# Performance work log

Hardware: AMD Instinct MI355X
Metric: run time of the kernel (lower is better)

Reference implementation:

```python
import jax, jax.numpy as jnp
import numpy as np

FG_FRACTION = 0.5
BATCHSIZE = 256
NUM_IMAGES = 1
NUM_CLASSES = 21
FG_THRESH = 0.5
BG_THRESH_HI = 0.5
BG_THRESH_LO = 0.1
ROIS_PER_IMAGE = BATCHSIZE // NUM_IMAGES                      # 256
FG_ROIS_PER_IMAGE = int(round(FG_FRACTION * ROIS_PER_IMAGE))  # 128
BG_ROIS_PER_IMAGE = ROIS_PER_IMAGE - FG_ROIS_PER_IMAGE        # 128


def _make_boxes(key, n, img=1000.0, max_wh=200.0):
    k1, k2 = jax.random.split(key)
    xy = jax.random.uniform(k1, (n, 2), dtype=jnp.float32) * (img - max_wh)
    wh = jax.random.uniform(k2, (n, 2), dtype=jnp.float32) * max_wh + 1.0
    return jnp.concatenate([xy, xy + wh], axis=1)  # valid [x1,y1,x2,y2]


def setup_inputs() -> dict:
    key = jax.random.key(0)
    k1, k2, k3 = jax.random.split(key, 3)
    N, G = 250000, 128
    rois = _make_boxes(k1, N)
    all_rois = jnp.concatenate([jnp.zeros((N, 1), jnp.float32), rois], axis=1)  # [N,5], col0 = image idx
    gt_boxes = _make_boxes(k2, G)                                               # [G,4]
    gt_labels = jax.random.randint(k3, (G,), 1, NUM_CLASSES).astype(jnp.int32)  # fg classes 1..20
    return {"all_rois": all_rois, "gt_boxes": gt_boxes, "gt_labels": gt_labels}


def _iou(a, b):
    area_a = (a[:, 2] - a[:, 0] + 1.0) * (a[:, 3] - a[:, 1] + 1.0)
    area_b = (b[:, 2] - b[:, 0] + 1.0) * (b[:, 3] - b[:, 1] + 1.0)
    ix1 = jnp.maximum(a[:, None, 0], b[None, :, 0])
    iy1 = jnp.maximum(a[:, None, 1], b[None, :, 1])
    ix2 = jnp.minimum(a[:, None, 2], b[None, :, 2])
    iy2 = jnp.minimum(a[:, None, 3], b[None, :, 3])
    iw = jnp.clip(ix2 - ix1 + 1.0, 0.0)
    ih = jnp.clip(iy2 - iy1 + 1.0, 0.0)
    inter = iw * ih
    return inter / (area_a[:, None] + area_b[None, :] - inter)


def _bbox_transform(ex, gt):
    ew = ex[:, 2] - ex[:, 0] + 1.0
    eh = ex[:, 3] - ex[:, 1] + 1.0
    ecx = ex[:, 0] + 0.5 * ew
    ecy = ex[:, 1] + 0.5 * eh
    gw = gt[:, 2] - gt[:, 0] + 1.0
    gh = gt[:, 3] - gt[:, 1] + 1.0
    gcx = gt[:, 0] + 0.5 * gw
    gcy = gt[:, 1] + 0.5 * gh
    return jnp.stack([(gcx - ecx) / ew, (gcy - ecy) / eh,
                      jnp.log(gw / ew), jnp.log(gh / eh)], axis=1)


def _proposal_target(all_rois, gt_boxes, gt_labels):
    G = gt_boxes.shape[0]
    # append gt boxes (with image-index 0 column) to the proposal set
    gt_rois = jnp.concatenate([jnp.zeros((G, 1), all_rois.dtype), gt_boxes], axis=1)
    all_rois = jnp.concatenate([all_rois, gt_rois], axis=0)          # [N+G, 5]

    overlaps = _iou(all_rois[:, 1:5], gt_boxes)                       # [N+G, G] -- dominant memory traffic
    gt_assignment = jnp.argmax(overlaps, axis=1)                      # [N+G]
    max_ov = jnp.max(overlaps, axis=1)                                # [N+G]
    labels_all = gt_labels[gt_assignment]                             # [N+G]

    fg_mask = max_ov >= FG_THRESH
    bg_mask = (max_ov < BG_THRESH_HI) & (max_ov >= BG_THRESH_LO)

    # random fg/bg sampling: top-k over random keys restricted to each mask
    u = jax.random.uniform(jax.random.key(42), (all_rois.shape[0],), dtype=jnp.float32)
    fg_idx = jax.lax.top_k(jnp.where(fg_mask, u, -1.0), FG_ROIS_PER_IMAGE)[1]
    bg_idx = jax.lax.top_k(jnp.where(bg_mask, u, -1.0), BG_ROIS_PER_IMAGE)[1]
    keep = jnp.concatenate([fg_idx, bg_idx])                          # [256]

    valid_fg = fg_mask[fg_idx]  # if fewer fg than requested, pad slots get label 0
    labels = jnp.concatenate([jnp.where(valid_fg, labels_all[fg_idx], 0),
                              jnp.zeros((BG_ROIS_PER_IMAGE,), labels_all.dtype)])

    rois = all_rois[keep]                                             # [256, 5]
    targets = _bbox_transform(rois[:, 1:5], gt_boxes[gt_assignment[keep]])  # [256, 4]

    # scatter targets into class-specific columns [256, 4*num_classes]
    onehot = jax.nn.one_hot(labels, NUM_CLASSES, dtype=targets.dtype)
    bbox_targets = (onehot[:, :, None] * targets[:, None, :]).reshape(ROIS_PER_IMAGE, 4 * NUM_CLASSES)
    bbox_targets = bbox_targets * (labels > 0)[:, None].astype(targets.dtype)
    return rois, labels, bbox_targets


def reference(all_rois, gt_boxes, gt_labels):
    return _proposal_target(all_rois, gt_boxes, gt_labels)
```

## Files before the change

kernel.cpp:

```cpp
#include <hip/hip_runtime.h>
#include <stdint.h>

#define GMAX 128
#define TK 128
#define NBINS 4096
#define CAND_MAX 4096
#define NUM_CLASSES 21
#define CBLOCK 1024
#define CBLOCKS 62

__device__ __forceinline__ void threefry2x32(uint32_t k0, uint32_t k1,
                                             uint32_t& x0, uint32_t& x1) {
  uint32_t ks0 = k0, ks1 = k1, ks2 = k0 ^ k1 ^ 0x1BD11BDAu;
  x0 += ks0; x1 += ks1;
#define TF_ROUND(r) { x0 += x1; x1 = (x1 << (r)) | (x1 >> (32 - (r))); x1 ^= x0; }
  TF_ROUND(13) TF_ROUND(15) TF_ROUND(26) TF_ROUND(6)
  x0 += ks1; x1 += ks2 + 1u;
  TF_ROUND(17) TF_ROUND(29) TF_ROUND(16) TF_ROUND(24)
  x0 += ks2; x1 += ks0 + 2u;
  TF_ROUND(13) TF_ROUND(15) TF_ROUND(26) TF_ROUND(6)
  x0 += ks0; x1 += ks1 + 3u;
  TF_ROUND(17) TF_ROUND(29) TF_ROUND(16) TF_ROUND(24)
  x0 += ks1; x1 += ks2 + 4u;
  TF_ROUND(13) TF_ROUND(15) TF_ROUND(26) TF_ROUND(6)
  x0 += ks2; x1 += ks0 + 5u;
#undef TF_ROUND
}

__global__ void __launch_bounds__(256)
score_kernel(const float* __restrict__ all_rois,
             const float* __restrict__ gt_boxes,
             uint32_t* __restrict__ score,
             uint32_t* __restrict__ hist,
             int N, int M, int G) {
  __shared__ float4 sbox[GMAX];
  __shared__ float  sga[GMAX];
  const int t = threadIdx.x;
  if (t < G) {
    float4 b = reinterpret_cast<const float4*>(gt_boxes)[t];
    sbox[t] = b;
    sga[t] = __fmul_rn(__fadd_rn(__fsub_rn(b.z, b.x), 1.0f),
                       __fadd_rn(__fsub_rn(b.w, b.y), 1.0f));
  }
  __syncthreads();
  const int i = blockIdx.x * 256 + t;
  if (i >= M) return;

  float bx1, by1, bx2, by2;
  if (i < N) {
    bx1 = all_rois[(size_t)i * 5 + 1];
    by1 = all_rois[(size_t)i * 5 + 2];
    bx2 = all_rois[(size_t)i * 5 + 3];
    by2 = all_rois[(size_t)i * 5 + 4];
  } else {
    float4 b = sbox[i - N];
    bx1 = b.x; by1 = b.y; bx2 = b.z; by2 = b.w;
  }
  const float area = __fmul_rn(__fadd_rn(__fsub_rn(bx2, bx1), 1.0f),
                               __fadd_rn(__fsub_rn(by2, by1), 1.0f));
  float best = -1.0f;
  int bi = 0;
  for (int g = 0; g < G; ++g) {
    float4 gb = sbox[g];
    float ix1 = fmaxf(bx1, gb.x);
    float iy1 = fmaxf(by1, gb.y);
    float ix2 = fminf(bx2, gb.z);
    float iy2 = fminf(by2, gb.w);
    float iw = fmaxf(__fadd_rn(__fsub_rn(ix2, ix1), 1.0f), 0.0f);
    float ih = fmaxf(__fadd_rn(__fsub_rn(iy2, iy1), 1.0f), 0.0f);
    float inter = __fmul_rn(iw, ih);
    float uni = __fsub_rn(__fadd_rn(area, sga[g]), inter);
    float ov = __fdiv_rn(inter, uni);
    if (ov > best) { best = ov; bi = g; }
  }

  uint32_t cx0 = 0u, cx1 = (uint32_t)i;
  threefry2x32(0u, 42u, cx0, cx1);
  uint32_t ubits = (cx0 ^ cx1) >> 9;

  uint32_t fg = (best >= 0.5f) ? 1u : 0u;
  uint32_t bg = (!fg && best >= 0.1f) ? 1u : 0u;
  score[i] = (ubits << 9) | ((uint32_t)bi << 2) | (fg << 1) | bg;
  if (fg)      atomicAdd(&hist[ubits >> 11], 1u);
  else if (bg) atomicAdd(&hist[NBINS + (ubits >> 11)], 1u);
}

__global__ void __launch_bounds__(CBLOCK)
compact_kernel(const uint32_t* __restrict__ score, int M,
               const uint32_t* __restrict__ hist,
               int* __restrict__ meta_cnt,
               uint64_t* __restrict__ cand) {
  __shared__ uint64_t gs[CBLOCK];
  __shared__ int s_jstar[2], s_bth[2];
  const int t = threadIdx.x;

  {
    const int b0 = 4 * t;
    uint64_t acc = 0;
    for (int k = 0; k < 4; ++k)
      acc += ((uint64_t)hist[b0 + k] << 32) | (uint64_t)hist[NBINS + b0 + k];
    gs[t] = acc;
    if (t < 2) s_jstar[t] = -1;
    __syncthreads();
    for (int d = 1; d < CBLOCK; d <<= 1) {
      uint64_t add = (t + d < CBLOCK) ? gs[t + d] : 0ull;
      __syncthreads();
      gs[t] += add;
      __syncthreads();
    }
    uint32_t vfg = (uint32_t)(gs[t] >> 32);
    uint32_t vbg = (uint32_t)gs[t];
    uint32_t nfg = (t < CBLOCK - 1) ? (uint32_t)(gs[t + 1] >> 32) : 0u;
    uint32_t nbg = (t < CBLOCK - 1) ? (uint32_t)gs[t + 1] : 0u;
    if (vfg >= (uint32_t)TK && (t == CBLOCK - 1 || nfg < (uint32_t)TK)) s_jstar[0] = t;
    if (vbg >= (uint32_t)TK && (t == CBLOCK - 1 || nbg < (uint32_t)TK)) s_jstar[1] = t;
    __syncthreads();
    if (t == 0) {
      for (int m = 0; m < 2; ++m) {
        int j = s_jstar[m], B = -1;
        if (j >= 0) {
          uint32_t base = 0;
          if (j < CBLOCK - 1)
            base = (m == 0) ? (uint32_t)(gs[j + 1] >> 32) : (uint32_t)gs[j + 1];
          const uint32_t* h = hist + m * NBINS;
          B = 4 * j;
          for (int b = 4 * j + 3; b >= 4 * j; --b) {
            base += h[b];
            if (base >= (uint32_t)TK) { B = b; break; }
          }
        }
        s_bth[m] = B;
      }
    }
    __syncthreads();
  }

  for (int i = blockIdx.x * CBLOCK + t; i < M; i += CBLOCKS * CBLOCK) {
    uint32_t s = score[i];
    uint32_t mb = s & 3u;
    if (!mb) continue;
    int m = (mb & 2u) ? 0 : 1;
    int B = s_bth[m];
    if (B >= 0 && (int)(s >> 20) < B) continue;
    int p = atomicAdd(&meta_cnt[m], 1);
    if (p < CAND_MAX)
      cand[(size_t)m * CAND_MAX + p] =
          (((uint64_t)((s >> 9) + 1u)) << 32) | (uint64_t)(~(uint32_t)i);
  }
}

__global__ void __launch_bounds__(1024)
final_kernel(const float* __restrict__ all_rois,
             const float* __restrict__ gt_boxes,
             const int* __restrict__ gt_labels,
             const uint32_t* __restrict__ score,
             const uint64_t* __restrict__ cand_g,
             const int* __restrict__ meta_cnt,
             float* __restrict__ out, int N, int M) {
  __shared__ uint64_t cand[CAND_MAX];
  __shared__ int keep[2 * TK];
  __shared__ int fgvalid[TK];
  __shared__ float s_tx[2 * TK], s_ty[2 * TK], s_tw[2 * TK], s_th[2 * TK];
  __shared__ int s_label[2 * TK];
  const int t = threadIdx.x;

  for (int m = 0; m < 2; ++m) {
    int cnt = meta_cnt[m]; if (cnt > CAND_MAX) cnt = CAND_MAX;
    int P = TK;
    while (P < cnt) P <<= 1;
    for (int p = t; p < P; p += 1024)
      cand[p] = (p < cnt) ? cand_g[(size_t)m * CAND_MAX + p] : 0ull;
    __syncthreads();
    for (int k = 2; k <= P; k <<= 1) {
      for (int j = k >> 1; j > 0; j >>= 1) {
        for (int idx = t; idx < P; idx += 1024) {
          int l = idx ^ j;
          if (l > idx) {
            uint64_t a = cand[idx], b = cand[l];
            bool swp = ((idx & k) == 0) ? (a < b) : (a > b);
            if (swp) { cand[idx] = b; cand[l] = a; }
          }
        }
        __syncthreads();
      }
    }
    if (cnt < TK && t == 0) {
      int fill = cnt;
      uint32_t mask_bit = (m == 0) ? 2u : 1u;
      for (int i = 0; i < M && fill < TK; ++i)
        if (!(score[i] & mask_bit)) cand[fill++] = (uint64_t)(~(uint32_t)i);
    }
    __syncthreads();
    if (t < TK) {
      uint64_t c = cand[t];
      keep[m * TK + t] = (int)(~(uint32_t)(c & 0xFFFFFFFFull));
      if (m == 0) fgvalid[t] = ((c >> 32) != 0ull) ? 1 : 0;
    }
    __syncthreads();
  }

  const int R = 2 * TK;
  float* rois_out   = out;
  float* labels_out = out + (size_t)R * 5;
  float* bt_out     = out + (size_t)R * 5 + R;

  if (t < R) {
    const int i = keep[t];
    float rimg, rx1, ry1, rx2, ry2;
    if (i < N) {
      rimg = all_rois[(size_t)i * 5 + 0];
      rx1  = all_rois[(size_t)i * 5 + 1];
      ry1  = all_rois[(size_t)i * 5 + 2];
      rx2  = all_rois[(size_t)i * 5 + 3];
      ry2  = all_rois[(size_t)i * 5 + 4];
    } else {
      int g = i - N;
      rimg = 0.0f;
      rx1 = gt_boxes[g * 4 + 0]; ry1 = gt_boxes[g * 4 + 1];
      rx2 = gt_boxes[g * 4 + 2]; ry2 = gt_boxes[g * 4 + 3];
    }
    rois_out[t * 5 + 0] = rimg;
    rois_out[t * 5 + 1] = rx1;
    rois_out[t * 5 + 2] = ry1;
    rois_out[t * 5 + 3] = rx2;
    rois_out[t * 5 + 4] = ry2;

    const int ga = (int)((score[i] >> 2) & 127u);
    int label = (t < TK && fgvalid[t]) ? gt_labels[ga] : 0;
    labels_out[t] = (float)label;
    s_label[t] = label;

    float gx1 = gt_boxes[ga * 4 + 0], gy1 = gt_boxes[ga * 4 + 1];
    float gx2 = gt_boxes[ga * 4 + 2], gy2 = gt_boxes[ga * 4 + 3];
    float ew = rx2 - rx1 + 1.0f, eh = ry2 - ry1 + 1.0f;
    float ecx = rx1 + 0.5f * ew, ecy = ry1 + 0.5f * eh;
    float gw = gx2 - gx1 + 1.0f, gh = gy2 - gy1 + 1.0f;
    float gcx = gx1 + 0.5f * gw, gcy = gy1 + 0.5f * gh;
    s_tx[t] = (gcx - ecx) / ew;
    s_ty[t] = (gcy - ecy) / eh;
    s_tw[t] = logf(gw / ew);
    s_th[t] = logf(gh / eh);
  }
  __syncthreads();

  const int TOT = R * 4 * NUM_CLASSES;
  for (int idx = t; idx < TOT; idx += 1024) {
    int r = idx / (4 * NUM_CLASSES);
    int c = idx - r * (4 * NUM_CLASSES);
    int lab = s_label[r];
    float v = 0.0f;
    if (lab > 0 && (c >> 2) == lab) {
      int cc = c & 3;
      v = (cc == 0) ? s_tx[r] : (cc == 1) ? s_ty[r] : (cc == 2) ? s_tw[r] : s_th[r];
    }
    bt_out[idx] = v;
  }
}

extern "C" void kernel_launch(void* const* d_in, const int* in_sizes, int n_in,
                              void* d_out, int out_size, void* d_ws, size_t ws_size,
                              hipStream_t stream) {
  const float* all_rois = (const float*)d_in[0];
  const float* gt_boxes = (const float*)d_in[1];
  const int*   gt_labels = (const int*)d_in[2];
  const int N = in_sizes[0] / 5;
  const int G = in_sizes[2];
  const int M = N + G;

  char* ws = (char*)d_ws;
  int* meta = (int*)ws;
  uint32_t* hist = (uint32_t*)(ws + 256);
  size_t off = 256 + (size_t)2 * NBINS * 4;
  uint32_t* score = (uint32_t*)(ws + off);
  off += (((size_t)M * 4) + 255) & ~(size_t)255;
  uint64_t* cand = (uint64_t*)(ws + off);
  float* out = (float*)d_out;

  hipMemsetAsync(ws, 0, 256 + (size_t)2 * NBINS * 4, stream);
  score_kernel<<<(M + 255) / 256, 256, 0, stream>>>(all_rois, gt_boxes, score,
                                                    hist, N, M, G);
  compact_kernel<<<CBLOCKS, CBLOCK, 0, stream>>>(score, M, hist, meta, cand);
  final_kernel<<<1, 1024, 0, stream>>>(all_rois, gt_boxes, gt_labels, score,
                                       cand, meta, out, N, M);
}
```

Baseline: 116.2 us.

## Fold histogram threshold into last score block; rank-select candidates instead of bitonic sort

The histogram prefix scan and threshold-bin search move out of the compact kernel into the last-finishing block of the score kernel, found through an atomic block counter, and the thresholds are written to global metadata. The compact kernel becomes a wide 256-thread grid that reads four scores per thread with vectorized loads and no per-block prologue scan. The final kernel replaces the shared-memory bitonic sort with a quadratic rank count per candidate, cutting the barrier-heavy sort passes. The trade-offs are an extra atomic and fence per score block and O(cnt^2) rank work, which relies on the candidate count staying small.

```diff
diff --git a/kernel.cpp b/kernel.cpp
--- a/kernel.cpp
+++ b/kernel.cpp
@@ -6,8 +6,6 @@
 #define NBINS 4096
 #define CAND_MAX 4096
 #define NUM_CLASSES 21
-#define CBLOCK 1024
-#define CBLOCKS 62
 
 __device__ __forceinline__ void threefry2x32(uint32_t k0, uint32_t k1,
                                              uint32_t& x0, uint32_t& x1) {
@@ -32,6 +30,7 @@
              const float* __restrict__ gt_boxes,
              uint32_t* __restrict__ score,
              uint32_t* __restrict__ hist,
+             int* __restrict__ meta,
              int N, int M, int G) {
   __shared__ float4 sbox[GMAX];
   __shared__ float  sga[GMAX];
@@ -44,108 +43,128 @@
   }
   __syncthreads();
   const int i = blockIdx.x * 256 + t;
-  if (i >= M) return;
-
-  float bx1, by1, bx2, by2;
-  if (i < N) {
-    bx1 = all_rois[(size_t)i * 5 + 1];
-    by1 = all_rois[(size_t)i * 5 + 2];
-    bx2 = all_rois[(size_t)i * 5 + 3];
-    by2 = all_rois[(size_t)i * 5 + 4];
+
+  if (i < M) {
+    float bx1, by1, bx2, by2;
+    if (i < N) {
+      bx1 = all_rois[(size_t)i * 5 + 1];
+      by1 = all_rois[(size_t)i * 5 + 2];
+      bx2 = all_rois[(size_t)i * 5 + 3];
+      by2 = all_rois[(size_t)i * 5 + 4];
+    } else {
+      float4 b = sbox[i - N];
+      bx1 = b.x; by1 = b.y; bx2 = b.z; by2 = b.w;
+    }
+    const float area = __fmul_rn(__fadd_rn(__fsub_rn(bx2, bx1), 1.0f),
+                                 __fadd_rn(__fsub_rn(by2, by1), 1.0f));
+    float best = -1.0f;
+    int bi = 0;
+    for (int g = 0; g < G; ++g) {
+      float4 gb = sbox[g];
+      float ix1 = fmaxf(bx1, gb.x);
+      float iy1 = fmaxf(by1, gb.y);
+      float ix2 = fminf(bx2, gb.z);
+      float iy2 = fminf(by2, gb.w);
+      float iw = fmaxf(__fadd_rn(__fsub_rn(ix2, ix1), 1.0f), 0.0f);
+      float ih = fmaxf(__fadd_rn(__fsub_rn(iy2, iy1), 1.0f), 0.0f);
+      float inter = __fmul_rn(iw, ih);
+      float uni = __fsub_rn(__fadd_rn(area, sga[g]), inter);
+      float ov = __fdiv_rn(inter, uni);
+      if (ov > best) { best = ov; bi = g; }
+    }
+
+    uint32_t cx0 = 0u, cx1 = (uint32_t)i;
+    threefry2x32(0u, 42u, cx0, cx1);
+    uint32_t ubits = (cx0 ^ cx1) >> 9;
+
+    uint32_t fg = (best >= 0.5f) ? 1u : 0u;
+    uint32_t bg = (!fg && best >= 0.1f) ? 1u : 0u;
+    score[i] = (ubits << 9) | ((uint32_t)bi << 2) | (fg << 1) | bg;
+    if (fg)      atomicAdd(&hist[ubits >> 11], 1u);
+    else if (bg) atomicAdd(&hist[NBINS + (ubits >> 11)], 1u);
+  }
+
+  __threadfence();
+  __shared__ unsigned s_prev;
+  if (t == 0) s_prev = atomicAdd((unsigned int*)&meta[2], 1u);
+  __syncthreads();
+  if (s_prev != gridDim.x - 1) return;
+  __threadfence();
+
+  __shared__ uint64_t gs[256];
+  __shared__ int s_jstar[2];
+  const int b0 = 16 * t;
+  uint64_t acc = 0;
+  for (int k = 0; k < 16; ++k) {
+    uint32_t hf = __hip_atomic_load(&hist[b0 + k], __ATOMIC_RELAXED,
+                                    __HIP_MEMORY_SCOPE_AGENT);
+    uint32_t hb = __hip_atomic_load(&hist[NBINS + b0 + k], __ATOMIC_RELAXED,
+                                    __HIP_MEMORY_SCOPE_AGENT);
+    acc += ((uint64_t)hf << 32) | (uint64_t)hb;
+  }
+  gs[t] = acc;
+  if (t < 2) s_jstar[t] = -1;
+  __syncthreads();
+  for (int d = 1; d < 256; d <<= 1) {
+    uint64_t add = (t + d < 256) ? gs[t + d] : 0ull;
+    __syncthreads();
+    gs[t] += add;
+    __syncthreads();
+  }
+  uint32_t vfg = (uint32_t)(gs[t] >> 32);
+  uint32_t vbg = (uint32_t)gs[t];
+  uint32_t nfg = (t < 255) ? (uint32_t)(gs[t + 1] >> 32) : 0u;
+  uint32_t nbg = (t < 255) ? (uint32_t)gs[t + 1] : 0u;
+  if (vfg >= (uint32_t)TK && (t == 255 || nfg < (uint32_t)TK)) s_jstar[0] = t;
+  if (vbg >= (uint32_t)TK && (t == 255 || nbg < (uint32_t)TK)) s_jstar[1] = t;
+  __syncthreads();
+  if (t == 0) {
+    for (int m = 0; m < 2; ++m) {
+      int j = s_jstar[m], B = -1;
+      if (j >= 0) {
+        uint32_t base = 0;
+        if (j < 255)
+          base = (m == 0) ? (uint32_t)(gs[j + 1] >> 32) : (uint32_t)gs[j + 1];
+        B = 16 * j;
+        for (int b = 16 * j + 15; b >= 16 * j; --b) {
+          base += __hip_atomic_load(&hist[m * NBINS + b], __ATOMIC_RELAXED,
+                                    __HIP_MEMORY_SCOPE_AGENT);
+          if (base >= (uint32_t)TK) { B = b; break; }
+        }
+      }
+      meta[4 + m] = B;
+    }
+  }
+}
+
+__global__ void __launch_bounds__(256)
+compact_kernel(const uint32_t* __restrict__ score, int M,
+               int* __restrict__ meta,
+               uint64_t* __restrict__ cand) {
+  const int bth[2] = {meta[4], meta[5]};
+  const int base = (blockIdx.x * 256 + threadIdx.x) * 4;
+  if (base >= M) return;
+  uint32_t ss[4];
+  int lim;
+  if (base + 3 < M) {
+    uint4 s4 = *reinterpret_cast<const uint4*>(score + base);
+    ss[0] = s4.x; ss[1] = s4.y; ss[2] = s4.z; ss[3] = s4.w;
+    lim = 4;
   } else {
-    float4 b = sbox[i - N];
-    bx1 = b.x; by1 = b.y; bx2 = b.z; by2 = b.w;
-  }
-  const float area = __fmul_rn(__fadd_rn(__fsub_rn(bx2, bx1), 1.0f),
-                               __fadd_rn(__fsub_rn(by2, by1), 1.0f));
-  float best = -1.0f;
-  int bi = 0;
-  for (int g = 0; g < G; ++g) {
-    float4 gb = sbox[g];
-    float ix1 = fmaxf(bx1, gb.x);
-    float iy1 = fmaxf(by1, gb.y);
-    float ix2 = fminf(bx2, gb.z);
-    float iy2 = fminf(by2, gb.w);
-    float iw = fmaxf(__fadd_rn(__fsub_rn(ix2, ix1), 1.0f), 0.0f);
-    float ih = fmaxf(__fadd_rn(__fsub_rn(iy2, iy1), 1.0f), 0.0f);
-    float inter = __fmul_rn(iw, ih);
-    float uni = __fsub_rn(__fadd_rn(area, sga[g]), inter);
-    float ov = __fdiv_rn(inter, uni);
-    if (ov > best) { best = ov; bi = g; }
-  }
-
-  uint32_t cx0 = 0u, cx1 = (uint32_t)i;
-  threefry2x32(0u, 42u, cx0, cx1);
-  uint32_t ubits = (cx0 ^ cx1) >> 9;
-
-  uint32_t fg = (best >= 0.5f) ? 1u : 0u;
-  uint32_t bg = (!fg && best >= 0.1f) ? 1u : 0u;
-  score[i] = (ubits << 9) | ((uint32_t)bi << 2) | (fg << 1) | bg;
-  if (fg)      atomicAdd(&hist[ubits >> 11], 1u);
-  else if (bg) atomicAdd(&hist[NBINS + (ubits >> 11)], 1u);
-}
-
-__global__ void __launch_bounds__(CBLOCK)
-compact_kernel(const uint32_t* __restrict__ score, int M,
-               const uint32_t* __restrict__ hist,
-               int* __restrict__ meta_cnt,
-               uint64_t* __restrict__ cand) {
-  __shared__ uint64_t gs[CBLOCK];
-  __shared__ int s_jstar[2], s_bth[2];
-  const int t = threadIdx.x;
-
-  {
-    const int b0 = 4 * t;
-    uint64_t acc = 0;
-    for (int k = 0; k < 4; ++k)
-      acc += ((uint64_t)hist[b0 + k] << 32) | (uint64_t)hist[NBINS + b0 + k];
-    gs[t] = acc;
-    if (t < 2) s_jstar[t] = -1;
-    __syncthreads();
-    for (int d = 1; d < CBLOCK; d <<= 1) {
-      uint64_t add = (t + d < CBLOCK) ? gs[t + d] : 0ull;
-      __syncthreads();
-      gs[t] += add;
-      __syncthreads();
-    }
-    uint32_t vfg = (uint32_t)(gs[t] >> 32);
-    uint32_t vbg = (uint32_t)gs[t];
-    uint32_t nfg = (t < CBLOCK - 1) ? (uint32_t)(gs[t + 1] >> 32) : 0u;
-    uint32_t nbg = (t < CBLOCK - 1) ? (uint32_t)gs[t + 1] : 0u;
-    if (vfg >= (uint32_t)TK && (t == CBLOCK - 1 || nfg < (uint32_t)TK)) s_jstar[0] = t;
-    if (vbg >= (uint32_t)TK && (t == CBLOCK - 1 || nbg < (uint32_t)TK)) s_jstar[1] = t;
-    __syncthreads();
-    if (t == 0) {
-      for (int m = 0; m < 2; ++m) {
-        int j = s_jstar[m], B = -1;
-        if (j >= 0) {
-          uint32_t base = 0;
-          if (j < CBLOCK - 1)
-            base = (m == 0) ? (uint32_t)(gs[j + 1] >> 32) : (uint32_t)gs[j + 1];
-          const uint32_t* h = hist + m * NBINS;
-          B = 4 * j;
-          for (int b = 4 * j + 3; b >= 4 * j; --b) {
-            base += h[b];
-            if (base >= (uint32_t)TK) { B = b; break; }
-          }
-        }
-        s_bth[m] = B;
-      }
-    }
-    __syncthreads();
-  }
-
-  for (int i = blockIdx.x * CBLOCK + t; i < M; i += CBLOCKS * CBLOCK) {
-    uint32_t s = score[i];
+    lim = M - base;
+    for (int k = 0; k < lim; ++k) ss[k] = score[base + k];
+  }
+  for (int k = 0; k < lim; ++k) {
+    uint32_t s = ss[k];
     uint32_t mb = s & 3u;
     if (!mb) continue;
     int m = (mb & 2u) ? 0 : 1;
-    int B = s_bth[m];
+    int B = bth[m];
     if (B >= 0 && (int)(s >> 20) < B) continue;
-    int p = atomicAdd(&meta_cnt[m], 1);
+    int p = atomicAdd(&meta[m], 1);
     if (p < CAND_MAX)
       cand[(size_t)m * CAND_MAX + p] =
-          (((uint64_t)((s >> 9) + 1u)) << 32) | (uint64_t)(~(uint32_t)i);
+          (((uint64_t)((s >> 9) + 1u)) << 32) | (uint64_t)(~(uint32_t)(base + k));
   }
 }
 
@@ -155,7 +174,7 @@
              const int* __restrict__ gt_labels,
              const uint32_t* __restrict__ score,
              const uint64_t* __restrict__ cand_g,
-             const int* __restrict__ meta_cnt,
+             const int* __restrict__ meta,
              float* __restrict__ out, int N, int M) {
   __shared__ uint64_t cand[CAND_MAX];
   __shared__ int keep[2 * TK];
@@ -165,36 +184,29 @@
   const int t = threadIdx.x;
 
   for (int m = 0; m < 2; ++m) {
-    int cnt = meta_cnt[m]; if (cnt > CAND_MAX) cnt = CAND_MAX;
-    int P = TK;
-    while (P < cnt) P <<= 1;
-    for (int p = t; p < P; p += 1024)
-      cand[p] = (p < cnt) ? cand_g[(size_t)m * CAND_MAX + p] : 0ull;
-    __syncthreads();
-    for (int k = 2; k <= P; k <<= 1) {
-      for (int j = k >> 1; j > 0; j >>= 1) {
-        for (int idx = t; idx < P; idx += 1024) {
-          int l = idx ^ j;
-          if (l > idx) {
-            uint64_t a = cand[idx], b = cand[l];
-            bool swp = ((idx & k) == 0) ? (a < b) : (a > b);
-            if (swp) { cand[idx] = b; cand[l] = a; }
-          }
-        }
-        __syncthreads();
+    int cnt = meta[m]; if (cnt > CAND_MAX) cnt = CAND_MAX;
+    for (int p = t; p < cnt; p += 1024)
+      cand[p] = cand_g[(size_t)m * CAND_MAX + p];
+    __syncthreads();
+    for (int p = t; p < cnt; p += 1024) {
+      uint64_t key = cand[p];
+      int r = 0;
+      for (int j = 0; j < cnt; ++j) r += (cand[j] > key) ? 1 : 0;
+      if (r < TK) {
+        keep[m * TK + r] = (int)(~(uint32_t)(key & 0xFFFFFFFFull));
+        if (m == 0) fgvalid[r] = 1;
       }
     }
+    __syncthreads();
     if (cnt < TK && t == 0) {
       int fill = cnt;
       uint32_t mask_bit = (m == 0) ? 2u : 1u;
-      for (int i = 0; i < M && fill < TK; ++i)
-        if (!(score[i] & mask_bit)) cand[fill++] = (uint64_t)(~(uint32_t)i);
-    }
-    __syncthreads();
-    if (t < TK) {
-      uint64_t c = cand[t];
-      keep[m * TK + t] = (int)(~(uint32_t)(c & 0xFFFFFFFFull));
-      if (m == 0) fgvalid[t] = ((c >> 32) != 0ull) ? 1 : 0;
+      for (int i2 = 0; i2 < M && fill < TK; ++i2)
+        if (!(score[i2] & mask_bit)) {
+          keep[m * TK + fill] = i2;
+          if (m == 0) fgvalid[fill] = 0;
+          fill++;
+        }
     }
     __syncthreads();
   }
@@ -278,8 +290,9 @@
 
   hipMemsetAsync(ws, 0, 256 + (size_t)2 * NBINS * 4, stream);
   score_kernel<<<(M + 255) / 256, 256, 0, stream>>>(all_rois, gt_boxes, score,
-                                                    hist, N, M, G);
-  compact_kernel<<<CBLOCKS, CBLOCK, 0, stream>>>(score, M, hist, meta, cand);
+                                                    hist, meta, N, M, G);
+  const int nb4 = ((M + 3) / 4 + 255) / 256;
+  compact_kernel<<<nb4, 256, 0, stream>>>(score, M, meta, cand);
   final_kernel<<<1, 1024, 0, stream>>>(all_rois, gt_boxes, gt_labels, score,
                                        cand, meta, out, N, M);
 }
```

Result: slower. 162.4 us (+39.7%).
